# Kernel optimization log

Measured on AMD Instinct MI355X. Metric: run time of the kernel, lower is better.

The kernel has to match this reference:

```python
import jax, jax.numpy as jnp
import numpy as np

K = 0.1
GAMMA = 1.0


def setup_inputs() -> dict:
    key = jax.random.key(0)
    k1, k2, k3, k4, k5 = jax.random.split(key, 5)
    N, M, D = 16384, 2048, 128
    # Points must lie inside the Poincare ball (0 < norm < 1) for acos/asin validity.
    x = jax.random.normal(k1, (N, D), dtype=jnp.float32)
    x = x / jnp.linalg.norm(x, axis=1, keepdims=True)
    x = x * jax.random.uniform(k2, (N, 1), minval=0.3, maxval=0.9, dtype=jnp.float32)
    p = jax.random.normal(k3, (M, D), dtype=jnp.float32)
    p = p / jnp.linalg.norm(p, axis=1, keepdims=True)
    p = p * jax.random.uniform(k4, (M, 1), minval=0.3, maxval=0.9, dtype=jnp.float32)
    labels = jax.random.randint(k5, (N,), 0, M)
    return {"x": x, "p": p, "labels": labels}


def reference(x, p, labels):
    N = x.shape[0]
    dot = x @ p.T                                   # [N, M], replaces NxMxD broadcast
    nx2 = jnp.sum(x * x, axis=1, keepdims=True)     # [N, 1] = ||x||^2
    np2 = jnp.sum(p * p, axis=1)                    # [M]    = ||p||^2
    np_norm = jnp.sqrt(np2)                         # [M]

    num = dot * (1.0 + np2) - np2 * (1.0 + nx2)     # [N, M]
    # Faithful to original: sum of squared pairwise distances over the BATCH axis (dim=0)
    # sum_i ||x_i - p_j||^2 = sum_i||x_i||^2 + N*||p_j||^2 - 2*(sum_i x_i)@p_j
    sum_sq_dist = jnp.sum(nx2) + N * np2 - 2.0 * (jnp.sum(x, axis=0) @ p.T)  # [M]
    den = np_norm * jnp.sqrt(sum_sq_dist) * jnp.sqrt(1.0 + np2 * nx2 - 2.0 * dot)  # [N, M]
    angle = jnp.arccos(num / den)                   # [N, M]

    psi = jnp.arcsin(K * (1.0 - np2) / np_norm)     # [M], broadcast over rows
    angles = jnp.maximum(0.0, angle - psi)          # [N, M]

    rows = jnp.arange(N)
    positive = angles[rows, labels]                 # [N]
    neg = jnp.maximum(0.0, GAMMA - angles)          # [N, M]
    negative = jnp.sum(neg, axis=1) - neg[rows, labels]  # exclude label column
    return jnp.mean(positive + negative)
```

## Files before the change

### kernel.cpp

```cpp
#include <hip/hip_runtime.h>
#include <math.h>

#define KCONST 0.1f
#define GAMMA_C 1.0f
#define D_DIM 128

typedef __attribute__((ext_vector_type(8))) short bf16x8;
typedef __attribute__((ext_vector_type(4))) float f32x4;

#define ASYNC_COPY16(gsrc, ldst)                                                  \
  __builtin_amdgcn_global_load_lds(                                               \
      (const __attribute__((address_space(1))) void*)(gsrc),                      \
      (__attribute__((address_space(3))) void*)(ldst), 16, 0, 0)

__device__ __forceinline__ unsigned short f2bf(float f) {
  unsigned int u = __float_as_uint(f);
  u += 0x7fffu + ((u >> 16) & 1u);
  return (unsigned short)(u >> 16);
}

__global__ void prep_x(const float* __restrict__ x, unsigned short* __restrict__ xb,
                       float* __restrict__ nx2p, float* __restrict__ pSumX,
                       float* __restrict__ pS2, float* __restrict__ out_zero, int N) {
  if (blockIdx.x == 0 && threadIdx.x == 0) *out_zero = 0.f;
  const int tid = threadIdx.x;
  const int l = tid & 63, w = tid >> 6;
  const int l16 = l & 15, sub = l >> 4;
  const int waveId = blockIdx.x * 4 + w;
  const float4* x4 = (const float4*)x;
  ushort4* xb4 = (ushort4*)xb;
  float4 c0 = {0.f, 0.f, 0.f, 0.f}, c1 = {0.f, 0.f, 0.f, 0.f};
  float s2 = 0.f;
#pragma unroll
  for (int it = 0; it < 4; ++it) {
    int row = (waveId + it * 1024) * 4 + sub;
    float4 v0 = x4[row * 32 + l16];
    float4 v1 = x4[row * 32 + 16 + l16];
    c0.x += v0.x; c0.y += v0.y; c0.z += v0.z; c0.w += v0.w;
    c1.x += v1.x; c1.y += v1.y; c1.z += v1.z; c1.w += v1.w;
    ushort4 b0, b1;
    b0.x = f2bf(v0.x); b0.y = f2bf(v0.y); b0.z = f2bf(v0.z); b0.w = f2bf(v0.w);
    b1.x = f2bf(v1.x); b1.y = f2bf(v1.y); b1.z = f2bf(v1.z); b1.w = f2bf(v1.w);
    xb4[row * 32 + l16] = b0;
    xb4[row * 32 + 16 + l16] = b1;
    float sq = v0.x * v0.x;
    sq = fmaf(v0.y, v0.y, sq); sq = fmaf(v0.z, v0.z, sq); sq = fmaf(v0.w, v0.w, sq);
    sq = fmaf(v1.x, v1.x, sq); sq = fmaf(v1.y, v1.y, sq);
    sq = fmaf(v1.z, v1.z, sq); sq = fmaf(v1.w, v1.w, sq);
    sq += __shfl_down(sq, 8); sq += __shfl_down(sq, 4);
    sq += __shfl_down(sq, 2); sq += __shfl_down(sq, 1);
    if (l16 == 0) {
      nx2p[row] = 1.f + sq;
      s2 += sq;
    }
  }
  s2 += __shfl_down(s2, 16);
  s2 += __shfl_down(s2, 32);
  __shared__ float cs[128];
  __shared__ float s2w[4];
  if (tid < 128) cs[tid] = 0.f;
  if (l == 0) s2w[w] = s2;
  __syncthreads();
  atomicAdd(&cs[l16 * 4 + 0], c0.x); atomicAdd(&cs[l16 * 4 + 1], c0.y);
  atomicAdd(&cs[l16 * 4 + 2], c0.z); atomicAdd(&cs[l16 * 4 + 3], c0.w);
  atomicAdd(&cs[64 + l16 * 4 + 0], c1.x); atomicAdd(&cs[64 + l16 * 4 + 1], c1.y);
  atomicAdd(&cs[64 + l16 * 4 + 2], c1.z); atomicAdd(&cs[64 + l16 * 4 + 3], c1.w);
  __syncthreads();
  if (tid < 128) pSumX[blockIdx.x * 128 + tid] = cs[tid];
  if (tid == 0) pS2[blockIdx.x] = s2w[0] + s2w[1] + s2w[2] + s2w[3];
}

__global__ void merge_sums(const float* __restrict__ pSumX, const float* __restrict__ pS2,
                           float* __restrict__ sum_x, float* __restrict__ sum_nx2) {
  __shared__ float seg[8][128];
  __shared__ float s2w[4];
  const int t = threadIdx.x;
  const int col = t & 127;
  const int sg = t >> 7;
  float s = 0.f;
#pragma unroll
  for (int b = 0; b < 32; ++b) s += pSumX[(sg * 32 + b) * 128 + col];
  seg[sg][col] = s;
  float s2 = (t < 256) ? pS2[t] : 0.f;
  if (t < 256) {
#pragma unroll
    for (int off = 32; off; off >>= 1) s2 += __shfl_down(s2, off);
    if ((t & 63) == 0) s2w[t >> 6] = s2;
  }
  __syncthreads();
  if (t < 128) {
    float r = 0.f;
#pragma unroll
    for (int k = 0; k < 8; ++k) r += seg[k][col];
    sum_x[t] = r;
  }
  if (t == 0) sum_nx2[0] = s2w[0] + s2w[1] + s2w[2] + s2w[3];
}

__global__ void prep_p(const float* __restrict__ p, unsigned short* __restrict__ pb,
                       const float* __restrict__ sum_x, const float* __restrict__ sum_nx2,
                       float4* __restrict__ colc, float* __restrict__ psiA,
                       int M, int N) {
  const int lane = threadIdx.x & 63;
  const int wave = threadIdx.x >> 6;
  const int j = blockIdx.x * 4 + wave;
  if (j >= M) return;
  const float2* p2 = (const float2*)p;
  ushort2* pb2 = (ushort2*)pb;
  float2 v = p2[j * 64 + lane];
  ushort2 b;
  b.x = f2bf(v.x);
  b.y = f2bf(v.y);
  pb2[j * 64 + lane] = b;
  float np2 = fmaf(v.x, v.x, v.y * v.y);
  float sd = fmaf(v.x, sum_x[2 * lane], v.y * sum_x[2 * lane + 1]);
#pragma unroll
  for (int off = 32; off; off >>= 1) {
    np2 += __shfl_down(np2, off);
    sd += __shfl_down(sd, off);
  }
  if (lane == 0) {
    float ssd = *sum_nx2 + (float)N * np2 - 2.f * sd;
    float npn = sqrtf(np2);
    float cfi = 1.f / (npn * sqrtf(ssd));
    float4 cc;
    cc.x = (1.f + np2) * cfi;
    cc.y = np2 * cfi;
    cc.z = np2;
    cc.w = np2 / (1.f + np2);
    colc[j] = cc;
    psiA[j] = asinf(KCONST * (1.f - np2) / npn);
  }
}

__global__ __launch_bounds__(256, 2) void pair_mfma(
    const unsigned short* __restrict__ xb, const unsigned short* __restrict__ pb,
    const int* __restrict__ labels, const float* __restrict__ nx2p,
    const float4* __restrict__ colc, const float* __restrict__ psiA,
    float* __restrict__ out, float invN) {
  __shared__ float4 xs4[2048];
  __shared__ float4 ps4[2][1024];
  __shared__ float wred[4];

  const int b = blockIdx.x;
  const int rowTile = b >> 2;
  const int cg = b & 3;
  const int row0 = rowTile * 128;

  const int tid = threadIdx.x;
  const int l = tid & 63;
  const int w = tid >> 6;
  const float4* xg = (const float4*)(xb + (size_t)row0 * D_DIM);

#pragma unroll
  for (int ci = w; ci < 32; ci += 4) {
    int qi = ci * 64 + l;
    int r = qi >> 4, ql = qi & 15;
    ASYNC_COPY16(xg + r * 16 + (ql ^ (r & 15)), xs4 + ci * 64);
  }
  {
    const float4* pg = (const float4*)(pb + (size_t)(cg * 8) * 64 * D_DIM);
#pragma unroll
    for (int ci = w; ci < 16; ci += 4) {
      int qi = ci * 64 + l;
      int r = qi >> 4, ql = qi & 15;
      ASYNC_COPY16(pg + r * 16 + (ql ^ (r & 15)), ps4[0] + ci * 64);
    }
  }

  const int m = tid & 15;
  const int q = (tid >> 4) & 3;
  const int wr = (w & 1) * 64;
  const int wc = (w >> 1) * 32;

  f32x4 rnp4v[4];
  int4 lb4v[4];
#pragma unroll
  for (int r = 0; r < 4; ++r) {
    rnp4v[r] = __builtin_bit_cast(f32x4, *(const float4*)&nx2p[row0 + wr + r * 16 + q * 4]);
    lb4v[r] = *(const int4*)&labels[row0 + wr + r * 16 + q * 4];
  }

  float4 ccur0 = colc[(cg * 8) * 64 + wc + m];
  float4 ccur1 = colc[(cg * 8) * 64 + wc + 16 + m];

  float ssum = 0.f;
#pragma unroll
  for (int it = 0; it < 8; ++it) {
    __syncthreads();
    const int cur = it & 1;
    if (it < 7) {
      const float4* pg = (const float4*)(pb + (size_t)(cg * 8 + it + 1) * 64 * D_DIM);
#pragma unroll
      for (int ci = w; ci < 16; ci += 4) {
        int qi = ci * 64 + l;
        int r = qi >> 4, ql = qi & 15;
        ASYNC_COPY16(pg + r * 16 + (ql ^ (r & 15)), ps4[cur ^ 1] + ci * 64);
      }
    }
    float4 cnext0, cnext1;
    if (it < 7) {
      cnext0 = colc[(cg * 8 + it + 1) * 64 + wc + m];
      cnext1 = colc[(cg * 8 + it + 1) * 64 + wc + 16 + m];
    }

    f32x4 acc[4][2];
#pragma unroll
    for (int r = 0; r < 4; ++r) {
      acc[r][0] = (f32x4)(0.f);
      acc[r][1] = (f32x4)(0.f);
    }
#pragma unroll
    for (int s = 0; s < 4; ++s) {
      const int qphys = (s * 4 + q) ^ m;
      bf16x8 a[4], bf[2];
#pragma unroll
      for (int c = 0; c < 2; ++c)
        bf[c] = __builtin_bit_cast(bf16x8, ps4[cur][(wc + c * 16 + m) * 16 + qphys]);
#pragma unroll
      for (int r = 0; r < 4; ++r)
        a[r] = __builtin_bit_cast(bf16x8, xs4[(wr + r * 16 + m) * 16 + qphys]);
#pragma unroll
      for (int r = 0; r < 4; ++r)
#pragma unroll
        for (int c = 0; c < 2; ++c)
          acc[r][c] = __builtin_amdgcn_mfma_f32_16x16x32_bf16(a[r], bf[c], acc[r][c], 0, 0, 0);
    }

    const int ct0 = (cg * 8 + it) * 64;
#pragma unroll
    for (int c = 0; c < 2; ++c) {
      const int col = ct0 + wc + c * 16 + m;
      const float4 cc = (c == 0) ? ccur0 : ccur1;
      const float Tc = cc.w;
#pragma unroll
      for (int r = 0; r < 4; ++r) {
        const f32x4 rnp4 = rnp4v[r];
        const int4 lb4 = lb4v[r];
        const f32x4 dv = acc[r][c];
        float e0 = fmaf(-Tc, rnp4[0], dv[0]);
        float e1 = fmaf(-Tc, rnp4[1], dv[1]);
        float e2 = fmaf(-Tc, rnp4[2], dv[2]);
        float e3 = fmaf(-Tc, rnp4[3], dv[3]);
        float hm = fmaxf(fmaxf(e0, e1), fmaxf(e2, e3));
        bool h = (hm > 0.f) | (col == lb4.x) | (col == lb4.y) |
                 (col == lb4.z) | (col == lb4.w);
        if (__builtin_expect(h, 0)) {
          const float psi = psiA[col];
          const float C1 = 1.f + psi;
          const float omnp2 = 1.f - cc.z;
#pragma unroll
          for (int g = 0; g < 4; ++g) {
            float rnp = rnp4[g];
            float dot = dv[g];
            int lb = (g == 0) ? lb4.x : (g == 1) ? lb4.y : (g == 2) ? lb4.z : lb4.w;
            float den2 = fmaf(cc.z, rnp, omnp2) - 2.f * dot;
            float nump = fmaf(dot, cc.x, -cc.y * rnp);
            float u = nump * __builtin_amdgcn_rsqf(den2);
            u = __builtin_amdgcn_fmed3f(u, -1.f, 1.f);
            float ax = fabsf(u);
            float rt = __builtin_amdgcn_sqrtf(1.f - ax);
            float poly = fmaf(fmaf(fmaf(-0.0187293f, ax, 0.0742610f), ax, -0.2121144f),
                              ax, 1.5707288f);
            float ac = rt * poly;
            ac = (u >= 0.f) ? ac : 3.14159265358979f - ac;
            float neg = __builtin_amdgcn_fmed3f(C1 - ac, 0.f, 1.f);
            float pos = fmaxf(0.f, ac - psi);
            ssum += (col == lb) ? pos : neg;
          }
        }
      }
    }
    if (it < 7) {
      ccur0 = cnext0;
      ccur1 = cnext1;
    }
  }

#pragma unroll
  for (int off = 32; off; off >>= 1) ssum += __shfl_down(ssum, off);
  if (l == 0) wred[w] = ssum;
  __syncthreads();
  if (tid == 0)
    atomicAdd(out, (wred[0] + wred[1] + wred[2] + wred[3]) * invN);
}

extern "C" void kernel_launch(void* const* d_in, const int* in_sizes, int n_in,
                              void* d_out, int out_size, void* d_ws, size_t ws_size,
                              hipStream_t stream) {
  const float* x = (const float*)d_in[0];
  const float* p = (const float*)d_in[1];
  const int* labels = (const int*)d_in[2];
  float* out = (float*)d_out;
  const int N = in_sizes[2];
  const int M = in_sizes[1] / D_DIM;

  float* ws = (float*)d_ws;
  float* nx2p = ws;
  float4* colc = (float4*)(ws + N);
  float* psiA = ws + N + 4 * M;
  unsigned short* xb = (unsigned short*)(ws + N + 5 * M);
  unsigned short* pb = (unsigned short*)(ws + N + 5 * M + 64 * N);
  float* pSumX = ws + N + 5 * M + 64 * N + 64 * M;
  float* pS2 = pSumX + 256 * 128;
  float* sum_x = pS2 + 256;
  float* sum_nx2 = sum_x + 128;

  prep_x<<<256, 256, 0, stream>>>(x, xb, nx2p, pSumX, pS2, out, N);
  merge_sums<<<1, 1024, 0, stream>>>(pSumX, pS2, sum_x, sum_nx2);
  prep_p<<<M / 4, 256, 0, stream>>>(p, pb, sum_x, sum_nx2, colc, psiA, M, N);

  pair_mfma<<<512, 256, 0, stream>>>(xb, pb, labels, nx2p, colc, psiA, out,
                                     1.0f / (float)N);
}
```

Before: 93.72 us.

## Switch pairwise dot products from bf16 to scaled fp8 MFMA

Converts x and p to fp8 with a scale of 16 instead of bf16, halving workspace, global traffic and LDS footprint, and uses the fp8 16x16x32 MFMA. The column constants are rescaled by 1/256 (and the threshold by 256) so the rest of the math sees the unscaled dot product. prep_p is rewritten so four rows share a wave, and pair_mfma's launch bounds are raised so more blocks can fit per CU. Using fp8 precision for the dot products risks accuracy in the arccos and the threshold test near boundaries.

```diff
diff --git a/kernel.cpp b/kernel.cpp
--- a/kernel.cpp
+++ b/kernel.cpp
@@ -5,7 +5,6 @@
 #define GAMMA_C 1.0f
 #define D_DIM 128
 
-typedef __attribute__((ext_vector_type(8))) short bf16x8;
 typedef __attribute__((ext_vector_type(4))) float f32x4;
 
 #define ASYNC_COPY16(gsrc, ldst)                                                  \
@@ -13,13 +12,16 @@
       (const __attribute__((address_space(1))) void*)(gsrc),                      \
       (__attribute__((address_space(3))) void*)(ldst), 16, 0, 0)
 
-__device__ __forceinline__ unsigned short f2bf(float f) {
-  unsigned int u = __float_as_uint(f);
-  u += 0x7fffu + ((u >> 16) & 1u);
-  return (unsigned short)(u >> 16);
-}
-
-__global__ void prep_x(const float* __restrict__ x, unsigned short* __restrict__ xb,
+#define FP8_SCALE 16.0f
+#define INV_TWO_OVER_SQ 0.0078125f
+
+__device__ __forceinline__ int pk_fp8x4(float a, float b, float c, float d) {
+  int v = __builtin_amdgcn_cvt_pk_fp8_f32(a, b, 0, 0);
+  v = __builtin_amdgcn_cvt_pk_fp8_f32(c, d, v, 1);
+  return v;
+}
+
+__global__ void prep_x(const float* __restrict__ x, unsigned char* __restrict__ xb,
                        float* __restrict__ nx2p, float* __restrict__ pSumX,
                        float* __restrict__ pS2, float* __restrict__ out_zero, int N) {
   if (blockIdx.x == 0 && threadIdx.x == 0) *out_zero = 0.f;
@@ -28,21 +30,19 @@
   const int l16 = l & 15, sub = l >> 4;
   const int waveId = blockIdx.x * 4 + w;
   const float4* x4 = (const float4*)x;
-  ushort4* xb4 = (ushort4*)xb;
   float4 c0 = {0.f, 0.f, 0.f, 0.f}, c1 = {0.f, 0.f, 0.f, 0.f};
   float s2 = 0.f;
 #pragma unroll
   for (int it = 0; it < 4; ++it) {
     int row = (waveId + it * 1024) * 4 + sub;
-    float4 v0 = x4[row * 32 + l16];
-    float4 v1 = x4[row * 32 + 16 + l16];
+    float4 v0 = x4[row * 32 + 2 * l16];
+    float4 v1 = x4[row * 32 + 2 * l16 + 1];
     c0.x += v0.x; c0.y += v0.y; c0.z += v0.z; c0.w += v0.w;
     c1.x += v1.x; c1.y += v1.y; c1.z += v1.z; c1.w += v1.w;
-    ushort4 b0, b1;
-    b0.x = f2bf(v0.x); b0.y = f2bf(v0.y); b0.z = f2bf(v0.z); b0.w = f2bf(v0.w);
-    b1.x = f2bf(v1.x); b1.y = f2bf(v1.y); b1.z = f2bf(v1.z); b1.w = f2bf(v1.w);
-    xb4[row * 32 + l16] = b0;
-    xb4[row * 32 + 16 + l16] = b1;
+    int2 st;
+    st.x = pk_fp8x4(v0.x * FP8_SCALE, v0.y * FP8_SCALE, v0.z * FP8_SCALE, v0.w * FP8_SCALE);
+    st.y = pk_fp8x4(v1.x * FP8_SCALE, v1.y * FP8_SCALE, v1.z * FP8_SCALE, v1.w * FP8_SCALE);
+    *(int2*)(xb + (size_t)row * 128 + 8 * l16) = st;
     float sq = v0.x * v0.x;
     sq = fmaf(v0.y, v0.y, sq); sq = fmaf(v0.z, v0.z, sq); sq = fmaf(v0.w, v0.w, sq);
     sq = fmaf(v1.x, v1.x, sq); sq = fmaf(v1.y, v1.y, sq);
@@ -61,10 +61,10 @@
   if (tid < 128) cs[tid] = 0.f;
   if (l == 0) s2w[w] = s2;
   __syncthreads();
-  atomicAdd(&cs[l16 * 4 + 0], c0.x); atomicAdd(&cs[l16 * 4 + 1], c0.y);
-  atomicAdd(&cs[l16 * 4 + 2], c0.z); atomicAdd(&cs[l16 * 4 + 3], c0.w);
-  atomicAdd(&cs[64 + l16 * 4 + 0], c1.x); atomicAdd(&cs[64 + l16 * 4 + 1], c1.y);
-  atomicAdd(&cs[64 + l16 * 4 + 2], c1.z); atomicAdd(&cs[64 + l16 * 4 + 3], c1.w);
+  atomicAdd(&cs[8 * l16 + 0], c0.x); atomicAdd(&cs[8 * l16 + 1], c0.y);
+  atomicAdd(&cs[8 * l16 + 2], c0.z); atomicAdd(&cs[8 * l16 + 3], c0.w);
+  atomicAdd(&cs[8 * l16 + 4], c1.x); atomicAdd(&cs[8 * l16 + 5], c1.y);
+  atomicAdd(&cs[8 * l16 + 6], c1.z); atomicAdd(&cs[8 * l16 + 7], c1.w);
   __syncthreads();
   if (tid < 128) pSumX[blockIdx.x * 128 + tid] = cs[tid];
   if (tid == 0) pS2[blockIdx.x] = s2w[0] + s2w[1] + s2w[2] + s2w[3];
@@ -97,49 +97,57 @@
   if (t == 0) sum_nx2[0] = s2w[0] + s2w[1] + s2w[2] + s2w[3];
 }
 
-__global__ void prep_p(const float* __restrict__ p, unsigned short* __restrict__ pb,
+__global__ void prep_p(const float* __restrict__ p, unsigned char* __restrict__ pb,
                        const float* __restrict__ sum_x, const float* __restrict__ sum_nx2,
                        float4* __restrict__ colc, float* __restrict__ psiA,
                        int M, int N) {
-  const int lane = threadIdx.x & 63;
-  const int wave = threadIdx.x >> 6;
-  const int j = blockIdx.x * 4 + wave;
-  if (j >= M) return;
-  const float2* p2 = (const float2*)p;
-  ushort2* pb2 = (ushort2*)pb;
-  float2 v = p2[j * 64 + lane];
-  ushort2 b;
-  b.x = f2bf(v.x);
-  b.y = f2bf(v.y);
-  pb2[j * 64 + lane] = b;
-  float np2 = fmaf(v.x, v.x, v.y * v.y);
-  float sd = fmaf(v.x, sum_x[2 * lane], v.y * sum_x[2 * lane + 1]);
-#pragma unroll
-  for (int off = 32; off; off >>= 1) {
+  const int tid = threadIdx.x;
+  const int l = tid & 63, w = tid >> 6;
+  const int l16 = l & 15, sub = l >> 4;
+  const int j = blockIdx.x * 16 + w * 4 + sub;
+  const float4* p4 = (const float4*)p;
+  float4 v0 = p4[j * 32 + 2 * l16];
+  float4 v1 = p4[j * 32 + 2 * l16 + 1];
+  int2 st;
+  st.x = pk_fp8x4(v0.x * FP8_SCALE, v0.y * FP8_SCALE, v0.z * FP8_SCALE, v0.w * FP8_SCALE);
+  st.y = pk_fp8x4(v1.x * FP8_SCALE, v1.y * FP8_SCALE, v1.z * FP8_SCALE, v1.w * FP8_SCALE);
+  *(int2*)(pb + (size_t)j * 128 + 8 * l16) = st;
+  float np2 = v0.x * v0.x;
+  np2 = fmaf(v0.y, v0.y, np2); np2 = fmaf(v0.z, v0.z, np2); np2 = fmaf(v0.w, v0.w, np2);
+  np2 = fmaf(v1.x, v1.x, np2); np2 = fmaf(v1.y, v1.y, np2);
+  np2 = fmaf(v1.z, v1.z, np2); np2 = fmaf(v1.w, v1.w, np2);
+  const float4 sx0 = *(const float4*)&sum_x[8 * l16];
+  const float4 sx1 = *(const float4*)&sum_x[8 * l16 + 4];
+  float sd = v0.x * sx0.x;
+  sd = fmaf(v0.y, sx0.y, sd); sd = fmaf(v0.z, sx0.z, sd); sd = fmaf(v0.w, sx0.w, sd);
+  sd = fmaf(v1.x, sx1.x, sd); sd = fmaf(v1.y, sx1.y, sd);
+  sd = fmaf(v1.z, sx1.z, sd); sd = fmaf(v1.w, sx1.w, sd);
+#pragma unroll
+  for (int off = 8; off; off >>= 1) {
     np2 += __shfl_down(np2, off);
     sd += __shfl_down(sd, off);
   }
-  if (lane == 0) {
+  if (l16 == 0) {
     float ssd = *sum_nx2 + (float)N * np2 - 2.f * sd;
     float npn = sqrtf(np2);
     float cfi = 1.f / (npn * sqrtf(ssd));
     float4 cc;
-    cc.x = (1.f + np2) * cfi;
+    cc.x = (1.f + np2) * cfi * (1.0f / 256.0f);
     cc.y = np2 * cfi;
     cc.z = np2;
-    cc.w = np2 / (1.f + np2);
+    cc.w = 256.0f * np2 / (1.f + np2);
     colc[j] = cc;
     psiA[j] = asinf(KCONST * (1.f - np2) / npn);
   }
 }
 
-__global__ __launch_bounds__(256, 2) void pair_mfma(
-    const unsigned short* __restrict__ xb, const unsigned short* __restrict__ pb,
+__global__ __launch_bounds__(256, 4) void pair_mfma(
+    const unsigned char* __restrict__ xb, const unsigned char* __restrict__ pb,
     const int* __restrict__ labels, const float* __restrict__ nx2p,
     const float4* __restrict__ colc, const float* __restrict__ psiA,
     float* __restrict__ out, float invN) {
-  __shared__ float4 xs4[2048];
-  __shared__ float4 ps4[2][1024];
+  __shared__ float4 xs4[1024];
+  __shared__ float4 ps4[2][512];
   __shared__ float wred[4];
 
   const int b = blockIdx.x;
@@ -150,21 +158,21 @@
   const int tid = threadIdx.x;
   const int l = tid & 63;
   const int w = tid >> 6;
-  const float4* xg = (const float4*)(xb + (size_t)row0 * D_DIM);
-
-#pragma unroll
-  for (int ci = w; ci < 32; ci += 4) {
+  const float4* xg = (const float4*)(xb + (size_t)row0 * 128);
+
+#pragma unroll
+  for (int ci = w; ci < 16; ci += 4) {
     int qi = ci * 64 + l;
-    int r = qi >> 4, ql = qi & 15;
-    ASYNC_COPY16(xg + r * 16 + (ql ^ (r & 15)), xs4 + ci * 64);
+    int r = qi >> 3, ql = qi & 7;
+    ASYNC_COPY16(xg + r * 8 + (ql ^ (r & 7)), xs4 + ci * 64);
   }
   {
-    const float4* pg = (const float4*)(pb + (size_t)(cg * 8) * 64 * D_DIM);
-#pragma unroll
-    for (int ci = w; ci < 16; ci += 4) {
+    const float4* pg = (const float4*)(pb + (size_t)(cg * 8) * 64 * 128);
+#pragma unroll
+    for (int ci = w; ci < 8; ci += 4) {
       int qi = ci * 64 + l;
-      int r = qi >> 4, ql = qi & 15;
-      ASYNC_COPY16(pg + r * 16 + (ql ^ (r & 15)), ps4[0] + ci * 64);
+      int r = qi >> 3, ql = qi & 7;
+      ASYNC_COPY16(pg + r * 8 + (ql ^ (r & 7)), ps4[0] + ci * 64);
     }
   }
 
@@ -184,18 +192,19 @@
   float4 ccur0 = colc[(cg * 8) * 64 + wc + m];
   float4 ccur1 = colc[(cg * 8) * 64 + wc + 16 + m];
 
+  const char* xsb = (const char*)xs4;
   float ssum = 0.f;
 #pragma unroll
   for (int it = 0; it < 8; ++it) {
     __syncthreads();
     const int cur = it & 1;
     if (it < 7) {
-      const float4* pg = (const float4*)(pb + (size_t)(cg * 8 + it + 1) * 64 * D_DIM);
-#pragma unroll
-      for (int ci = w; ci < 16; ci += 4) {
+      const float4* pg = (const float4*)(pb + (size_t)(cg * 8 + it + 1) * 64 * 128);
+#pragma unroll
+      for (int ci = w; ci < 8; ci += 4) {
         int qi = ci * 64 + l;
-        int r = qi >> 4, ql = qi & 15;
-        ASYNC_COPY16(pg + r * 16 + (ql ^ (r & 15)), ps4[cur ^ 1] + ci * 64);
+        int r = qi >> 3, ql = qi & 7;
+        ASYNC_COPY16(pg + r * 8 + (ql ^ (r & 7)), ps4[cur ^ 1] + ci * 64);
       }
     }
     float4 cnext0, cnext1;
@@ -204,6 +213,7 @@
       cnext1 = colc[(cg * 8 + it + 1) * 64 + wc + 16 + m];
     }
 
+    const char* psb = (const char*)ps4[cur];
     f32x4 acc[4][2];
 #pragma unroll
     for (int r = 0; r < 4; ++r) {
@@ -212,19 +222,24 @@
     }
 #pragma unroll
     for (int s = 0; s < 4; ++s) {
-      const int qphys = (s * 4 + q) ^ m;
-      bf16x8 a[4], bf[2];
-#pragma unroll
-      for (int c = 0; c < 2; ++c)
-        bf[c] = __builtin_bit_cast(bf16x8, ps4[cur][(wc + c * 16 + m) * 16 + qphys]);
+      const int g = s * 4 + q;
+      const int gq = g >> 1, gh = (g & 1) << 3;
+      long a[4], bf[2];
+#pragma unroll
+      for (int c = 0; c < 2; ++c) {
+        const int row = wc + c * 16 + m;
+        bf[c] = *(const long*)(psb + row * 128 + ((gq ^ (row & 7)) << 4) + gh);
+      }
+#pragma unroll
+      for (int r = 0; r < 4; ++r) {
+        const int row = wr + r * 16 + m;
+        a[r] = *(const long*)(xsb + row * 128 + ((gq ^ (row & 7)) << 4) + gh);
+      }
 #pragma unroll
       for (int r = 0; r < 4; ++r)
-        a[r] = __builtin_bit_cast(bf16x8, xs4[(wr + r * 16 + m) * 16 + qphys]);
-#pragma unroll
-      for (int r = 0; r < 4; ++r)
 #pragma unroll
         for (int c = 0; c < 2; ++c)
-          acc[r][c] = __builtin_amdgcn_mfma_f32_16x16x32_bf16(a[r], bf[c], acc[r][c], 0, 0, 0);
+          acc[r][c] = __builtin_amdgcn_mfma_f32_16x16x32_fp8_fp8(a[r], bf[c], acc[r][c], 0, 0, 0);
     }
 
     const int ct0 = (cg * 8 + it) * 64;
@@ -250,12 +265,12 @@
           const float C1 = 1.f + psi;
           const float omnp2 = 1.f - cc.z;
 #pragma unroll
-          for (int g = 0; g < 4; ++g) {
-            float rnp = rnp4[g];
-            float dot = dv[g];
-            int lb = (g == 0) ? lb4.x : (g == 1) ? lb4.y : (g == 2) ? lb4.z : lb4.w;
-            float den2 = fmaf(cc.z, rnp, omnp2) - 2.f * dot;
-            float nump = fmaf(dot, cc.x, -cc.y * rnp);
+          for (int g2 = 0; g2 < 4; ++g2) {
+            float rnp = rnp4[g2];
+            float dotRaw = dv[g2];
+            int lb = (g2 == 0) ? lb4.x : (g2 == 1) ? lb4.y : (g2 == 2) ? lb4.z : lb4.w;
+            float den2 = fmaf(-INV_TWO_OVER_SQ, dotRaw, fmaf(cc.z, rnp, omnp2));
+            float nump = fmaf(dotRaw, cc.x, -cc.y * rnp);
             float u = nump * __builtin_amdgcn_rsqf(den2);
             u = __builtin_amdgcn_fmed3f(u, -1.f, 1.f);
             float ax = fabsf(u);
@@ -299,16 +314,16 @@
   float* nx2p = ws;
   float4* colc = (float4*)(ws + N);
   float* psiA = ws + N + 4 * M;
-  unsigned short* xb = (unsigned short*)(ws + N + 5 * M);
-  unsigned short* pb = (unsigned short*)(ws + N + 5 * M + 64 * N);
-  float* pSumX = ws + N + 5 * M + 64 * N + 64 * M;
+  unsigned char* xb = (unsigned char*)(ws + N + 5 * M);
+  unsigned char* pb = (unsigned char*)(ws + N + 5 * M + 32 * N);
+  float* pSumX = ws + N + 5 * M + 32 * N + 32 * M;
   float* pS2 = pSumX + 256 * 128;
   float* sum_x = pS2 + 256;
   float* sum_nx2 = sum_x + 128;
 
   prep_x<<<256, 256, 0, stream>>>(x, xb, nx2p, pSumX, pS2, out, N);
   merge_sums<<<1, 1024, 0, stream>>>(pSumX, pS2, sum_x, sum_nx2);
-  prep_p<<<M / 4, 256, 0, stream>>>(p, pb, sum_x, sum_nx2, colc, psiA, M, N);
+  prep_p<<<M / 16, 256, 0, stream>>>(p, pb, sum_x, sum_nx2, colc, psiA, M, N);
 
   pair_mfma<<<512, 256, 0, stream>>>(xb, pb, labels, nx2p, colc, psiA, out,
                                      1.0f / (float)N);
```

After: 93.28 us. No clear change (-0.5%).
